# Optimization experiments

Hardware: AMD Instinct MI355X
Metric: run time of the kernel (lower is better)

The kernel has to match this reference:

```python
import jax, jax.numpy as jnp
import numpy as np

D_MODEL = 1024
NUM_HEADS = 16
NUM_KV_HEADS = 4
HEAD_DIM = D_MODEL // NUM_HEADS  # 64
KV_DIM = HEAD_DIM * NUM_KV_HEADS  # 256
B, N = 2, 2048


def setup_inputs() -> dict:
    key = jax.random.key(0)
    ks = jax.random.split(key, 7)
    std = 1.0 / np.sqrt(D_MODEL)
    return {
        "x": jax.random.normal(ks[0], (B, N, D_MODEL), dtype=jnp.float32),
        "cos": jax.random.uniform(ks[1], (N, HEAD_DIM // 2), dtype=jnp.float32),
        "sin": jax.random.uniform(ks[2], (N, HEAD_DIM // 2), dtype=jnp.float32),
        "Wq": jax.random.normal(ks[3], (D_MODEL, D_MODEL), dtype=jnp.float32) * std,
        "Wk": jax.random.normal(ks[4], (D_MODEL, KV_DIM), dtype=jnp.float32) * std,
        "Wv": jax.random.normal(ks[5], (D_MODEL, KV_DIM), dtype=jnp.float32) * std,
        "Wo": jax.random.normal(ks[6], (D_MODEL, D_MODEL), dtype=jnp.float32) * std,
    }


def _rope(t, cos, sin):
    # t: [B, H, N, head_dim]; cos/sin: [N, head_dim//2]
    t1, t2 = t[..., ::2], t[..., 1::2]
    c = cos[None, None]
    s = sin[None, None]
    # NOTE: halves are concatenated (not re-interleaved), faithful to source.
    return jnp.concatenate([t1 * c - t2 * s, t1 * s + t2 * c], axis=-1)


def reference(x, cos, sin, Wq, Wk, Wv, Wo):
    b, n, d = x.shape
    scale = HEAD_DIM ** -0.5
    q = (x @ Wq).reshape(b, n, NUM_HEADS, HEAD_DIM).transpose(0, 2, 1, 3)
    k = (x @ Wk).reshape(b, n, NUM_KV_HEADS, HEAD_DIM).transpose(0, 2, 1, 3)
    v = (x @ Wv).reshape(b, n, NUM_KV_HEADS, HEAD_DIM).transpose(0, 2, 1, 3)
    q = _rope(q, cos, sin)
    k = _rope(k, cos, sin)
    num_rep = NUM_HEADS // NUM_KV_HEADS
    k = jnp.repeat(k, num_rep, axis=1)  # [b, H, n, hd]
    v = jnp.repeat(v, num_rep, axis=1)
    attn = jnp.einsum("bhqd,bhkd->bhqk", q, k) * scale
    attn = jax.nn.softmax(attn, axis=-1)
    out = jnp.einsum("bhqk,bhkd->bhqd", attn, v)
    out = out.transpose(0, 2, 1, 3).reshape(b, n, d)
    return out @ Wo
```

## Files before the change

kernel.cpp:

```cpp
#include <hip/hip_runtime.h>
#include <math.h>

#define D_MODEL 1024
#define NHEADS  16
#define NKV     4
#define HDIM    64
#define KVDIM   256
#define BB      2
#define NN      2048
#define MROWS   (BB*NN)
#define QKVN    1536
#define NTASK   (MROWS*NHEADS)
#define NSPLIT  4

typedef unsigned short ushort_t;
typedef unsigned int uint_t;
typedef float    f32x4 __attribute__((ext_vector_type(4)));
typedef _Float16 h16x8 __attribute__((ext_vector_type(8)));
typedef __fp16   fp16x2 __attribute__((ext_vector_type(2)));

#define MFMAH(A,B,C) __builtin_amdgcn_mfma_f32_16x16x32_f16((A),(B),(C),0,0,0)

#define GLDS(gp, lp) __builtin_amdgcn_global_load_lds( \
    (const __attribute__((address_space(1))) void*)(gp), \
    (__attribute__((address_space(3))) void*)(lp), 16, 0, 0)

__device__ __forceinline__ ushort_t f2h(float f) {
    _Float16 h = (_Float16)f;
    return *(ushort_t*)&h;
}
__device__ __forceinline__ float h2f(ushort_t u) {
    return (float)(*(const _Float16*)&u);
}
__device__ __forceinline__ uint_t pk2h(float a, float b) {
    fp16x2 v = __builtin_amdgcn_cvt_pkrtz(a, b);
    return *(uint_t*)&v;
}

__global__ __launch_bounds__(256)
void cast_kernel(const float* __restrict__ src, ushort_t* __restrict__ dst, int n4)
{
    int i = blockIdx.x * 256 + threadIdx.x;
    if (i >= n4) return;
    float4 v = ((const float4*)src)[i];
    uint2 o;
    o.x = pk2h(v.x, v.y);
    o.y = pk2h(v.z, v.w);
    ((uint2*)dst)[i] = o;
}

__global__ __launch_bounds__(256)
void transpose_cast(const float* __restrict__ src, ushort_t* __restrict__ dst,
                    int K, int N)
{
    __shared__ float T[32][33];
    const int tx = threadIdx.x & 31, ty = threadIdx.x >> 5;
    const int n0 = blockIdx.x * 32, k0 = blockIdx.y * 32;
#pragma unroll
    for (int i = 0; i < 4; i++)
        T[ty + i * 8][tx] = src[(size_t)(k0 + ty + i * 8) * N + n0 + tx];
    __syncthreads();
#pragma unroll
    for (int i = 0; i < 4; i++)
        dst[(size_t)(n0 + ty + i * 8) * K + k0 + tx] = f2h(T[tx][ty + i * 8]);
}

__global__ __launch_bounds__(256)
void vtrans_kernel(const ushort_t* __restrict__ QKVh, ushort_t* __restrict__ Vt)
{
    __shared__ ushort_t T[32][34];
    const int tx = threadIdx.x & 31, ty = threadIdx.x >> 5;
    const int n0 = blockIdx.x * 32, d0 = blockIdx.y * 32, b = blockIdx.z;
#pragma unroll
    for (int i = 0; i < 4; i++)
        T[ty + i * 8][tx] =
            QKVh[(size_t)(b * NN + n0 + ty + i * 8) * QKVN + 1280 + d0 + tx];
    __syncthreads();
#pragma unroll
    for (int i = 0; i < 4; i++)
        Vt[(size_t)(b * 256 + d0 + ty + i * 8) * NN + n0 + tx] = T[tx][ty + i * 8];
}

#define NQW (MROWS*NHEADS*32)
#define NKW (MROWS*NKV*32)
__global__ __launch_bounds__(256)
void rope_kernel(const ushort_t* __restrict__ QKVh, const float* __restrict__ Cos,
                 const float* __restrict__ Sin, ushort_t* __restrict__ Qb,
                 ushort_t* __restrict__ Kb)
{
    const float SC = 0.125f * 1.44269504f;
    int idx = blockIdx.x * 256 + threadIdx.x;
    if (idx < NQW) {
        const int row = idx >> 9, rem = idx & 511;
        const int h = rem >> 5, j = rem & 31;
        const int b = row >> 11, n = row & (NN - 1);
        const uint_t pr = *(const uint_t*)&QKVh[(size_t)row * QKVN + h * 64 + 2 * j];
        const float e = h2f((ushort_t)pr), o = h2f((ushort_t)(pr >> 16));
        const float c = Cos[n * 32 + j], s = Sin[n * 32 + j];
        ushort_t* dst = Qb + ((size_t)(b * 16 + h) * NN + n) * 64;
        dst[j]      = f2h((e * c - o * s) * SC);
        dst[j + 32] = f2h((e * s + o * c) * SC);
    } else {
        const int i2 = idx - NQW;
        const int row = i2 >> 7, rem = i2 & 127;
        const int h = rem >> 5, j = rem & 31;
        const int b = row >> 11, n = row & (NN - 1);
        const uint_t pr = *(const uint_t*)&QKVh[(size_t)row * QKVN + 1024 + h * 64 + 2 * j];
        const float e = h2f((ushort_t)pr), o = h2f((ushort_t)(pr >> 16));
        const float c = Cos[n * 32 + j], s = Sin[n * 32 + j];
        ushort_t* dst = Kb + ((size_t)(b * 4 + h) * NN + n) * 64;
        dst[j]      = f2h(e * c - o * s);
        dst[j + 32] = f2h(e * s + o * c);
    }
}

__global__ __launch_bounds__(256)
void gemm_bt(const ushort_t* __restrict__ A, const ushort_t* __restrict__ Bt,
             void* __restrict__ C, int M, int N, int K, int halfout)
{
    __shared__ ushort_t As[2][128 * 32];
    __shared__ ushort_t Bs[2][64 * 32];

    const int tid  = threadIdx.x;
    const int wave = tid >> 6, lane = tid & 63;
    const int quad = lane >> 4, l16 = lane & 15;
    const int rowBase = blockIdx.y * 128, colBase = blockIdx.x * 64;
    const int wm = (wave >> 1) * 64, wn = (wave & 1) * 32;

    f32x4 acc[4][2];
    const f32x4 zz = {0.f, 0.f, 0.f, 0.f};
#pragma unroll
    for (int i = 0; i < 4; i++)
#pragma unroll
        for (int j = 0; j < 2; j++) acc[i][j] = zz;

    const int sr = wave * 32 + (lane >> 2);
    const int sc = ((lane & 3) ^ ((lane >> 3) & 3)) * 8;
    const ushort_t* Ag0 = A + (size_t)(rowBase + sr) * K + sc;
    const ushort_t* Ag1 = A + (size_t)(rowBase + sr + 16) * K + sc;
    const int segA0 = (wave * 2 + 0) * 512, segA1 = (wave * 2 + 1) * 512;
    const int br = wave * 16 + (lane >> 2);
    const ushort_t* Bg0 = Bt + (size_t)(colBase + br) * K + sc;
    const int segB = wave * 512;

    const int fcol = (quad ^ ((l16 >> 1) & 3)) * 8;

    GLDS(Ag0, &As[0][segA0]);
    GLDS(Ag1, &As[0][segA1]);
    GLDS(Bg0, &Bs[0][segB]);

    for (int k0 = 0; k0 < K; k0 += 32) {
        const int cur = (k0 >> 5) & 1, nxt = cur ^ 1;
        __syncthreads();
        if (k0 + 32 < K) {
            GLDS(Ag0 + k0 + 32, &As[nxt][segA0]);
            GLDS(Ag1 + k0 + 32, &As[nxt][segA1]);
            GLDS(Bg0 + k0 + 32, &Bs[nxt][segB]);
        }

        h16x8 af[4], bf[2];
#pragma unroll
        for (int mt = 0; mt < 4; mt++)
            af[mt] = *(const h16x8*)&As[cur][(wm + mt * 16 + l16) * 32 + fcol];
#pragma unroll
        for (int nt = 0; nt < 2; nt++)
            bf[nt] = *(const h16x8*)&Bs[cur][(wn + nt * 16 + l16) * 32 + fcol];
#pragma unroll
        for (int mt = 0; mt < 4; mt++)
#pragma unroll
            for (int nt = 0; nt < 2; nt++)
                acc[mt][nt] = MFMAH(af[mt], bf[nt], acc[mt][nt]);
    }

    if (halfout) {
        ushort_t* Ch = (ushort_t*)C;
#pragma unroll
        for (int mt = 0; mt < 4; mt++)
#pragma unroll
            for (int nt = 0; nt < 2; nt++) {
                const int row = rowBase + wm + mt * 16 + quad * 4;
                const int col = colBase + wn + nt * 16 + l16;
#pragma unroll
                for (int r = 0; r < 4; r++)
                    Ch[(size_t)(row + r) * N + col] = f2h(acc[mt][nt][r]);
            }
    } else {
        float* Cf = (float*)C;
#pragma unroll
        for (int mt = 0; mt < 4; mt++)
#pragma unroll
            for (int nt = 0; nt < 2; nt++) {
                const int row = rowBase + wm + mt * 16 + quad * 4;
                const int col = colBase + wn + nt * 16 + l16;
#pragma unroll
                for (int r = 0; r < 4; r++)
                    Cf[(size_t)(row + r) * N + col] = acc[mt][nt][r];
            }
    }
}

__global__ __launch_bounds__(256)
void attn_mfma(const ushort_t* __restrict__ Qb, const ushort_t* __restrict__ Kb,
               const ushort_t* __restrict__ Vt, ushort_t* __restrict__ Pnum,
               float* __restrict__ Pl)
{
    const int qt = blockIdx.x, h = blockIdx.y;
    const int b = blockIdx.z >> 2, chunk = blockIdx.z & 3;
    const int kvh = h >> 2;
    const int tid = threadIdx.x;
    const int wave = tid >> 6, lane = tid & 63;
    const int quad = lane >> 4, l16 = lane & 15;

    __shared__ ushort_t Ks[64][72];
    __shared__ ushort_t Vs[64][72];
    __shared__ ushort_t Ps[4][16 * 72];
    ushort_t* ps = &Ps[wave][0];

    const int row0 = qt * 256 + wave * 64;
    h16x8 qf[4][2];
#pragma unroll
    for (int mt = 0; mt < 4; mt++) {
        const ushort_t* qp =
            Qb + ((size_t)(b * 16 + h) * NN + row0 + mt * 16 + l16) * 64 + quad * 8;
        qf[mt][0] = *(const h16x8*)qp;
        qf[mt][1] = *(const h16x8*)(qp + 32);
    }

    const ushort_t* kbase = Kb + (size_t)(b * 4 + kvh) * NN * 64;
    const ushort_t* vbase = Vt + (size_t)(b * 256 + kvh * 64) * NN;
    const int key_lo = chunk * (NN / NSPLIT);
    const int rot = (qt + ((h & 3) << 1)) & 7;

    const int srow = tid >> 2, sseg = (tid & 3) * 8;

    const f32x4 zz = {0.f, 0.f, 0.f, 0.f};
    f32x4 o[4][4];
#pragma unroll
    for (int mt = 0; mt < 4; mt++)
#pragma unroll
        for (int dt = 0; dt < 4; dt++) o[mt][dt] = zz;
    float lacc[4] = {0.f, 0.f, 0.f, 0.f};

    int key0 = key_lo + rot * 64;
    const ushort_t* kp0 = kbase + (size_t)(key0 + srow) * 64 + sseg;
    const ushort_t* vp0 = vbase + (size_t)srow * NN + key0 + sseg;
    uint4 kreg0 = *(const uint4*)kp0;
    uint4 kreg1 = *(const uint4*)(kp0 + 32);
    uint4 vreg0 = *(const uint4*)vp0;
    uint4 vreg1 = *(const uint4*)(vp0 + 32);

    for (int t = 0; t < 8; t++) {
        __syncthreads();
        *(uint4*)&Ks[srow][sseg]      = kreg0;
        *(uint4*)&Ks[srow][sseg + 32] = kreg1;
        *(uint4*)&Vs[srow][sseg]      = vreg0;
        *(uint4*)&Vs[srow][sseg + 32] = vreg1;
        __syncthreads();

        if (t < 7) {
            const int kn = key_lo + ((rot + t + 1) & 7) * 64;
            const ushort_t* kpn = kbase + (size_t)(kn + srow) * 64 + sseg;
            const ushort_t* vpn = vbase + (size_t)srow * NN + kn + sseg;
            kreg0 = *(const uint4*)kpn;
            kreg1 = *(const uint4*)(kpn + 32);
            vreg0 = *(const uint4*)vpn;
            vreg1 = *(const uint4*)(vpn + 32);
        }

        uint2 pkreg[4][4];
#pragma unroll
        for (int kt = 0; kt < 4; kt++) {
            h16x8 kf0 = *(const h16x8*)&Ks[kt * 16 + l16][quad * 8];
            h16x8 kf1 = *(const h16x8*)&Ks[kt * 16 + l16][32 + quad * 8];
#pragma unroll
            for (int mt = 0; mt < 4; mt++) {
                f32x4 st = MFMAH(kf0, qf[mt][0], zz);
                st = MFMAH(kf1, qf[mt][1], st);
                const float p0 = exp2f(st[0]);
                const float p1 = exp2f(st[1]);
                const float p2 = exp2f(st[2]);
                const float p3 = exp2f(st[3]);
                lacc[mt] += (p0 + p1) + (p2 + p3);
                pkreg[kt][mt].x = pk2h(p0, p1);
                pkreg[kt][mt].y = pk2h(p2, p3);
            }
        }

        h16x8 vf[4][2];
#pragma unroll
        for (int dt = 0; dt < 4; dt++) {
            vf[dt][0] = *(const h16x8*)&Vs[dt * 16 + l16][quad * 8];
            vf[dt][1] = *(const h16x8*)&Vs[dt * 16 + l16][32 + quad * 8];
        }
#pragma unroll
        for (int mt = 0; mt < 4; mt++) {
#pragma unroll
            for (int kt = 0; kt < 4; kt++)
                *(uint2*)&ps[l16 * 72 + kt * 16 + quad * 4] = pkreg[kt][mt];
            h16x8 pa0 = *(const h16x8*)&ps[l16 * 72 + quad * 8];
            h16x8 pa1 = *(const h16x8*)&ps[l16 * 72 + 32 + quad * 8];
#pragma unroll
            for (int dt = 0; dt < 4; dt++) {
                o[mt][dt] = MFMAH(vf[dt][0], pa0, o[mt][dt]);
                o[mt][dt] = MFMAH(vf[dt][1], pa1, o[mt][dt]);
            }
        }
    }

#pragma unroll
    for (int mt = 0; mt < 4; mt++) {
        lacc[mt] += __shfl_xor(lacc[mt], 16, 64);
        lacc[mt] += __shfl_xor(lacc[mt], 32, 64);
    }

    const size_t task0 = (size_t)(b * 16 + h) * NN + row0;
    ushort_t* np = Pnum + ((size_t)chunk * NTASK + task0) * 64;
#pragma unroll
    for (int mt = 0; mt < 4; mt++) {
        const float inv = 1.0f / lacc[mt];
#pragma unroll
        for (int dt = 0; dt < 4; dt++) {
            f32x4 v = o[mt][dt];
            uint2 pk;
            pk.x = pk2h(v[0] * inv, v[1] * inv);
            pk.y = pk2h(v[2] * inv, v[3] * inv);
            *(uint2*)&np[(size_t)(mt * 16 + l16) * 64 + dt * 16 + quad * 4] = pk;
        }
        if (quad == 0)
            Pl[(size_t)chunk * NTASK + task0 + mt * 16 + l16] = lacc[mt];
    }
}

__global__ __launch_bounds__(256)
void attn_combine(const ushort_t* __restrict__ Pnum, const float* __restrict__ Pl,
                  ushort_t* __restrict__ Ob)
{
    const int gid  = blockIdx.x * 256 + threadIdx.x;
    const int task = gid >> 4;
    const int d    = (gid & 15) * 4;
    float a0 = 0.f, a1 = 0.f, a2 = 0.f, a3 = 0.f, lsum = 0.f;
#pragma unroll
    for (int s = 0; s < NSPLIT; s++) {
        const uint2 pk = *(const uint2*)&Pnum[((size_t)s * NTASK + task) * 64 + d];
        const float l = Pl[(size_t)s * NTASK + task];
        const fp16x2 lo = *(const fp16x2*)&pk.x;
        const fp16x2 hi = *(const fp16x2*)&pk.y;
        a0 += l * (float)lo.x; a1 += l * (float)lo.y;
        a2 += l * (float)hi.x; a3 += l * (float)hi.y;
        lsum += l;
    }
    const float inv = 1.0f / lsum;
    const int n = task & (NN - 1), bh = task >> 11;
    const int h = bh & (NHEADS - 1), b = bh >> 4;
    ushort_t* op = Ob + (size_t)(b * NN + n) * D_MODEL + h * 64 + d;
    uint2 o2;
    o2.x = pk2h(a0 * inv, a1 * inv);
    o2.y = pk2h(a2 * inv, a3 * inv);
    *(uint2*)op = o2;
}

extern "C" void kernel_launch(void* const* d_in, const int* in_sizes, int n_in,
                              void* d_out, int out_size, void* d_ws, size_t ws_size,
                              hipStream_t stream)
{
    const float* x    = (const float*)d_in[0];
    const float* cosp = (const float*)d_in[1];
    const float* sinp = (const float*)d_in[2];
    const float* Wq   = (const float*)d_in[3];
    const float* Wk   = (const float*)d_in[4];
    const float* Wv   = (const float*)d_in[5];
    const float* Wo   = (const float*)d_in[6];

    char* w = (char*)d_ws;
    ushort_t* xb     = (ushort_t*)w;                       w += (size_t)MROWS * D_MODEL * 2;
    ushort_t* WqkvT  = (ushort_t*)w;                       w += (size_t)QKVN * D_MODEL * 2;
    ushort_t* WoT    = (ushort_t*)w;                       w += (size_t)D_MODEL * D_MODEL * 2;
    ushort_t* QKVh   = (ushort_t*)w;                       w += (size_t)MROWS * QKVN * 2;
    ushort_t* Qbuf   = (ushort_t*)w;                       w += (size_t)MROWS * D_MODEL * 2;
    ushort_t* Kbuf   = (ushort_t*)w;                       w += (size_t)MROWS * KVDIM * 2;
    ushort_t* Vt     = (ushort_t*)w;                       w += (size_t)MROWS * KVDIM * 2;
    ushort_t* Obuf   = (ushort_t*)w;                       w += (size_t)MROWS * D_MODEL * 2;
    ushort_t* Pnum   = (ushort_t*)w;                       w += (size_t)NSPLIT * NTASK * 64 * 2;
    float*    Pl     = (float*)w;

    cast_kernel<<<(MROWS * D_MODEL / 4 + 255) / 256, 256, 0, stream>>>(
        x, xb, MROWS * D_MODEL / 4);
    transpose_cast<<<dim3(D_MODEL / 32, D_MODEL / 32), 256, 0, stream>>>(
        Wq, WqkvT, D_MODEL, D_MODEL);
    transpose_cast<<<dim3(KVDIM / 32, D_MODEL / 32), 256, 0, stream>>>(
        Wk, WqkvT + (size_t)1024 * D_MODEL, D_MODEL, KVDIM);
    transpose_cast<<<dim3(KVDIM / 32, D_MODEL / 32), 256, 0, stream>>>(
        Wv, WqkvT + (size_t)1280 * D_MODEL, D_MODEL, KVDIM);
    transpose_cast<<<dim3(D_MODEL / 32, D_MODEL / 32), 256, 0, stream>>>(
        Wo, WoT, D_MODEL, D_MODEL);

    gemm_bt<<<dim3(QKVN / 64, MROWS / 128), 256, 0, stream>>>(
        xb, WqkvT, QKVh, MROWS, QKVN, D_MODEL, 1);

    rope_kernel<<<(NQW + NKW) / 256, 256, 0, stream>>>(QKVh, cosp, sinp, Qbuf, Kbuf);
    vtrans_kernel<<<dim3(NN / 32, KVDIM / 32, BB), 256, 0, stream>>>(QKVh, Vt);

    attn_mfma<<<dim3(NN / 256, NHEADS, BB * NSPLIT), 256, 0, stream>>>(
        Qbuf, Kbuf, Vt, Pnum, Pl);
    attn_combine<<<(NTASK * 16) / 256, 256, 0, stream>>>(Pnum, Pl, Obuf);

    gemm_bt<<<dim3(D_MODEL / 64, MROWS / 128), 256, 0, stream>>>(
        Obuf, WoT, d_out, MROWS, D_MODEL, D_MODEL, 0);
}
```

Measured before the change: 216.6 us.

## Fuse split-KV combine into Wo GEMM, merge prep kernels, halve KV splits

Merges the five cast and transpose launches into one prep kernel dispatched by block index. Halves the split-KV count, so each attention block covers twice as many keys and there are half as many partial outputs. Removes the separate combine kernel and the O buffer: the Wo GEMM now loads both partial numerators and their weights, normalizes and converts them to fp16 in registers, and stores the result into padded shared memory as its A tile. This cuts launch overhead and an intermediate round trip through global memory, at the cost of less attention parallelism and redundant combine work repeated across the GEMM's column blocks.

```diff
diff --git a/kernel.cpp b/kernel.cpp
--- a/kernel.cpp
+++ b/kernel.cpp
@@ -11,7 +11,7 @@
 #define MROWS   (BB*NN)
 #define QKVN    1536
 #define NTASK   (MROWS*NHEADS)
-#define NSPLIT  4
+#define NSPLIT  2
 
 typedef unsigned short ushort_t;
 typedef unsigned int uint_t;
@@ -38,31 +38,37 @@
 }
 
 __global__ __launch_bounds__(256)
-void cast_kernel(const float* __restrict__ src, ushort_t* __restrict__ dst, int n4)
-{
-    int i = blockIdx.x * 256 + threadIdx.x;
-    if (i >= n4) return;
-    float4 v = ((const float4*)src)[i];
-    uint2 o;
-    o.x = pk2h(v.x, v.y);
-    o.y = pk2h(v.z, v.w);
-    ((uint2*)dst)[i] = o;
-}
-
-__global__ __launch_bounds__(256)
-void transpose_cast(const float* __restrict__ src, ushort_t* __restrict__ dst,
-                    int K, int N)
+void prep_kernel(const float* __restrict__ x, const float* __restrict__ Wq,
+                 const float* __restrict__ Wk, const float* __restrict__ Wv,
+                 const float* __restrict__ Wo, ushort_t* __restrict__ xb,
+                 ushort_t* __restrict__ WqkvT, ushort_t* __restrict__ WoT)
 {
     __shared__ float T[32][33];
+    int blk = blockIdx.x;
+    if (blk < 4096) {
+        const int i = blk * 256 + threadIdx.x;
+        float4 v = ((const float4*)x)[i];
+        uint2 o;
+        o.x = pk2h(v.x, v.y);
+        o.y = pk2h(v.z, v.w);
+        ((uint2*)xb)[i] = o;
+        return;
+    }
+    blk -= 4096;
+    const float* src; ushort_t* dst; int N, bx, by;
+    if (blk < 1024)      { src = Wq; dst = WqkvT;                            N = D_MODEL; bx = blk & 31; by = blk >> 5; }
+    else if (blk < 1280) { blk -= 1024; src = Wk; dst = WqkvT + (size_t)1024 * D_MODEL; N = KVDIM; bx = blk & 7; by = blk >> 3; }
+    else if (blk < 1536) { blk -= 1280; src = Wv; dst = WqkvT + (size_t)1280 * D_MODEL; N = KVDIM; bx = blk & 7; by = blk >> 3; }
+    else                 { blk -= 1536; src = Wo; dst = WoT;                 N = D_MODEL; bx = blk & 31; by = blk >> 5; }
     const int tx = threadIdx.x & 31, ty = threadIdx.x >> 5;
-    const int n0 = blockIdx.x * 32, k0 = blockIdx.y * 32;
+    const int n0 = bx * 32, k0 = by * 32;
 #pragma unroll
     for (int i = 0; i < 4; i++)
         T[ty + i * 8][tx] = src[(size_t)(k0 + ty + i * 8) * N + n0 + tx];
     __syncthreads();
 #pragma unroll
     for (int i = 0; i < 4; i++)
-        dst[(size_t)(n0 + ty + i * 8) * K + k0 + tx] = f2h(T[tx][ty + i * 8]);
+        dst[(size_t)(n0 + ty + i * 8) * D_MODEL + k0 + tx] = f2h(T[tx][ty + i * 8]);
 }
 
 __global__ __launch_bounds__(256)
@@ -115,8 +121,8 @@
 }
 
 __global__ __launch_bounds__(256)
-void gemm_bt(const ushort_t* __restrict__ A, const ushort_t* __restrict__ Bt,
-             void* __restrict__ C, int M, int N, int K, int halfout)
+void gemm_qkv(const ushort_t* __restrict__ A, const ushort_t* __restrict__ Bt,
+              ushort_t* __restrict__ C, int M, int N, int K)
 {
     __shared__ ushort_t As[2][128 * 32];
     __shared__ ushort_t Bs[2][64 * 32];
@@ -172,31 +178,16 @@
                 acc[mt][nt] = MFMAH(af[mt], bf[nt], acc[mt][nt]);
     }
 
-    if (halfout) {
-        ushort_t* Ch = (ushort_t*)C;
-#pragma unroll
-        for (int mt = 0; mt < 4; mt++)
-#pragma unroll
-            for (int nt = 0; nt < 2; nt++) {
-                const int row = rowBase + wm + mt * 16 + quad * 4;
-                const int col = colBase + wn + nt * 16 + l16;
-#pragma unroll
-                for (int r = 0; r < 4; r++)
-                    Ch[(size_t)(row + r) * N + col] = f2h(acc[mt][nt][r]);
-            }
-    } else {
-        float* Cf = (float*)C;
-#pragma unroll
-        for (int mt = 0; mt < 4; mt++)
-#pragma unroll
-            for (int nt = 0; nt < 2; nt++) {
-                const int row = rowBase + wm + mt * 16 + quad * 4;
-                const int col = colBase + wn + nt * 16 + l16;
-#pragma unroll
-                for (int r = 0; r < 4; r++)
-                    Cf[(size_t)(row + r) * N + col] = acc[mt][nt][r];
-            }
-    }
+#pragma unroll
+    for (int mt = 0; mt < 4; mt++)
+#pragma unroll
+        for (int nt = 0; nt < 2; nt++) {
+            const int row = rowBase + wm + mt * 16 + quad * 4;
+            const int col = colBase + wn + nt * 16 + l16;
+#pragma unroll
+            for (int r = 0; r < 4; r++)
+                C[(size_t)(row + r) * N + col] = f2h(acc[mt][nt][r]);
+        }
 }
 
 __global__ __launch_bounds__(256)
@@ -205,7 +196,7 @@
                float* __restrict__ Pl)
 {
     const int qt = blockIdx.x, h = blockIdx.y;
-    const int b = blockIdx.z >> 2, chunk = blockIdx.z & 3;
+    const int b = blockIdx.z >> 1, chunk = blockIdx.z & 1;
     const int kvh = h >> 2;
     const int tid = threadIdx.x;
     const int wave = tid >> 6, lane = tid & 63;
@@ -229,7 +220,7 @@
     const ushort_t* kbase = Kb + (size_t)(b * 4 + kvh) * NN * 64;
     const ushort_t* vbase = Vt + (size_t)(b * 256 + kvh * 64) * NN;
     const int key_lo = chunk * (NN / NSPLIT);
-    const int rot = (qt + ((h & 3) << 1)) & 7;
+    const int rot = (qt + ((h & 3) << 2)) & 15;
 
     const int srow = tid >> 2, sseg = (tid & 3) * 8;
 
@@ -249,7 +240,7 @@
     uint4 vreg0 = *(const uint4*)vp0;
     uint4 vreg1 = *(const uint4*)(vp0 + 32);
 
-    for (int t = 0; t < 8; t++) {
+    for (int t = 0; t < 16; t++) {
         __syncthreads();
         *(uint4*)&Ks[srow][sseg]      = kreg0;
         *(uint4*)&Ks[srow][sseg + 32] = kreg1;
@@ -257,8 +248,8 @@
         *(uint4*)&Vs[srow][sseg + 32] = vreg1;
         __syncthreads();
 
-        if (t < 7) {
-            const int kn = key_lo + ((rot + t + 1) & 7) * 64;
+        if (t < 15) {
+            const int kn = key_lo + ((rot + t + 1) & 15) * 64;
             const ushort_t* kpn = kbase + (size_t)(kn + srow) * 64 + sseg;
             const ushort_t* vpn = vbase + (size_t)srow * NN + kn + sseg;
             kreg0 = *(const uint4*)kpn;
@@ -332,31 +323,114 @@
 }
 
 __global__ __launch_bounds__(256)
-void attn_combine(const ushort_t* __restrict__ Pnum, const float* __restrict__ Pl,
-                  ushort_t* __restrict__ Ob)
-{
-    const int gid  = blockIdx.x * 256 + threadIdx.x;
-    const int task = gid >> 4;
-    const int d    = (gid & 15) * 4;
-    float a0 = 0.f, a1 = 0.f, a2 = 0.f, a3 = 0.f, lsum = 0.f;
-#pragma unroll
-    for (int s = 0; s < NSPLIT; s++) {
-        const uint2 pk = *(const uint2*)&Pnum[((size_t)s * NTASK + task) * 64 + d];
-        const float l = Pl[(size_t)s * NTASK + task];
-        const fp16x2 lo = *(const fp16x2*)&pk.x;
-        const fp16x2 hi = *(const fp16x2*)&pk.y;
-        a0 += l * (float)lo.x; a1 += l * (float)lo.y;
-        a2 += l * (float)hi.x; a3 += l * (float)hi.y;
-        lsum += l;
-    }
-    const float inv = 1.0f / lsum;
-    const int n = task & (NN - 1), bh = task >> 11;
-    const int h = bh & (NHEADS - 1), b = bh >> 4;
-    ushort_t* op = Ob + (size_t)(b * NN + n) * D_MODEL + h * 64 + d;
-    uint2 o2;
-    o2.x = pk2h(a0 * inv, a1 * inv);
-    o2.y = pk2h(a2 * inv, a3 * inv);
-    *(uint2*)op = o2;
+void gemm_wo(const ushort_t* __restrict__ Pnum, const float* __restrict__ Pl,
+             const ushort_t* __restrict__ WoT, float* __restrict__ C)
+{
+    __shared__ ushort_t As[2][128 * 40];
+    __shared__ ushort_t Bs[2][64 * 32];
+
+    const int tid  = threadIdx.x;
+    const int wave = tid >> 6, lane = tid & 63;
+    const int quad = lane >> 4, l16 = lane & 15;
+    const int rowBase = blockIdx.y * 128, colBase = blockIdx.x * 64;
+    const int wm = (wave >> 1) * 64, wn = (wave & 1) * 32;
+
+    f32x4 acc[4][2];
+    const f32x4 zz = {0.f, 0.f, 0.f, 0.f};
+#pragma unroll
+    for (int i = 0; i < 4; i++)
+#pragma unroll
+        for (int j = 0; j < 2; j++) acc[i][j] = zz;
+
+    const int r0 = tid >> 2;
+    const int c8 = (tid & 3) * 8;
+    const int bB = rowBase >> 11;
+    const int n0 = (rowBase & (NN - 1)) + r0;
+
+    const int br = wave * 16 + (lane >> 2);
+    const int sc = ((lane & 3) ^ ((lane >> 3) & 3)) * 8;
+    const ushort_t* Bg0 = WoT + (size_t)(colBase + br) * D_MODEL + sc;
+    const int segB = wave * 512;
+    const int fcol = (quad ^ ((l16 >> 1) & 3)) * 8;
+
+    uint4 a0c0, a0c1, a1c0, a1c1;
+    float l00, l01, l10, l11;
+#define PREFA(k0) { \
+        const int h_ = (k0) >> 6; \
+        const int d_ = ((k0) & 63) + c8; \
+        const size_t t0_ = ((size_t)(bB * 16 + h_) << 11) + n0; \
+        const size_t t1_ = t0_ + 64; \
+        a0c0 = *(const uint4*)&Pnum[t0_ * 64 + d_]; \
+        a0c1 = *(const uint4*)&Pnum[((size_t)NTASK + t0_) * 64 + d_]; \
+        a1c0 = *(const uint4*)&Pnum[t1_ * 64 + d_]; \
+        a1c1 = *(const uint4*)&Pnum[((size_t)NTASK + t1_) * 64 + d_]; \
+        l00 = Pl[t0_]; l01 = Pl[NTASK + t0_]; \
+        l10 = Pl[t1_]; l11 = Pl[NTASK + t1_]; \
+    }
+
+    PREFA(0);
+    GLDS(Bg0, &Bs[0][segB]);
+
+    for (int k0 = 0; k0 < D_MODEL; k0 += 32) {
+        const int cur = (k0 >> 5) & 1, nxt = cur ^ 1;
+        __syncthreads();
+
+        {
+            const float i0 = 1.f / (l00 + l01), w00 = l00 * i0, w01 = l01 * i0;
+            const float i1 = 1.f / (l10 + l11), w10 = l10 * i1, w11 = l11 * i1;
+            uint4 o0, o1;
+            const uint_t* p0 = (const uint_t*)&a0c0;
+            const uint_t* p1 = (const uint_t*)&a0c1;
+            const uint_t* q0 = (const uint_t*)&a1c0;
+            const uint_t* q1 = (const uint_t*)&a1c1;
+            uint_t* po = (uint_t*)&o0;
+            uint_t* qo = (uint_t*)&o1;
+#pragma unroll
+            for (int j = 0; j < 4; j++) {
+                fp16x2 u = *(const fp16x2*)&p0[j];
+                fp16x2 v = *(const fp16x2*)&p1[j];
+                po[j] = pk2h(w00 * (float)u.x + w01 * (float)v.x,
+                             w00 * (float)u.y + w01 * (float)v.y);
+                fp16x2 s = *(const fp16x2*)&q0[j];
+                fp16x2 r = *(const fp16x2*)&q1[j];
+                qo[j] = pk2h(w10 * (float)s.x + w11 * (float)r.x,
+                             w10 * (float)s.y + w11 * (float)r.y);
+            }
+            *(uint4*)&As[cur][r0 * 40 + c8]        = o0;
+            *(uint4*)&As[cur][(r0 + 64) * 40 + c8] = o1;
+        }
+        __syncthreads();
+
+        if (k0 + 32 < D_MODEL) {
+            GLDS(Bg0 + k0 + 32, &Bs[nxt][segB]);
+            PREFA(k0 + 32);
+        }
+
+        h16x8 af[4], bf[2];
+#pragma unroll
+        for (int mt = 0; mt < 4; mt++)
+            af[mt] = *(const h16x8*)&As[cur][(wm + mt * 16 + l16) * 40 + quad * 8];
+#pragma unroll
+        for (int nt = 0; nt < 2; nt++)
+            bf[nt] = *(const h16x8*)&Bs[cur][(wn + nt * 16 + l16) * 32 + fcol];
+#pragma unroll
+        for (int mt = 0; mt < 4; mt++)
+#pragma unroll
+            for (int nt = 0; nt < 2; nt++)
+                acc[mt][nt] = MFMAH(af[mt], bf[nt], acc[mt][nt]);
+    }
+#undef PREFA
+
+#pragma unroll
+    for (int mt = 0; mt < 4; mt++)
+#pragma unroll
+        for (int nt = 0; nt < 2; nt++) {
+            const int row = rowBase + wm + mt * 16 + quad * 4;
+            const int col = colBase + wn + nt * 16 + l16;
+#pragma unroll
+            for (int r = 0; r < 4; r++)
+                C[(size_t)(row + r) * D_MODEL + col] = acc[mt][nt][r];
+        }
 }
 
 extern "C" void kernel_launch(void* const* d_in, const int* in_sizes, int n_in,
@@ -379,31 +453,20 @@
     ushort_t* Qbuf   = (ushort_t*)w;                       w += (size_t)MROWS * D_MODEL * 2;
     ushort_t* Kbuf   = (ushort_t*)w;                       w += (size_t)MROWS * KVDIM * 2;
     ushort_t* Vt     = (ushort_t*)w;                       w += (size_t)MROWS * KVDIM * 2;
-    ushort_t* Obuf   = (ushort_t*)w;                       w += (size_t)MROWS * D_MODEL * 2;
     ushort_t* Pnum   = (ushort_t*)w;                       w += (size_t)NSPLIT * NTASK * 64 * 2;
     float*    Pl     = (float*)w;
 
-    cast_kernel<<<(MROWS * D_MODEL / 4 + 255) / 256, 256, 0, stream>>>(
-        x, xb, MROWS * D_MODEL / 4);
-    transpose_cast<<<dim3(D_MODEL / 32, D_MODEL / 32), 256, 0, stream>>>(
-        Wq, WqkvT, D_MODEL, D_MODEL);
-    transpose_cast<<<dim3(KVDIM / 32, D_MODEL / 32), 256, 0, stream>>>(
-        Wk, WqkvT + (size_t)1024 * D_MODEL, D_MODEL, KVDIM);
-    transpose_cast<<<dim3(KVDIM / 32, D_MODEL / 32), 256, 0, stream>>>(
-        Wv, WqkvT + (size_t)1280 * D_MODEL, D_MODEL, KVDIM);
-    transpose_cast<<<dim3(D_MODEL / 32, D_MODEL / 32), 256, 0, stream>>>(
-        Wo, WoT, D_MODEL, D_MODEL);
-
-    gemm_bt<<<dim3(QKVN / 64, MROWS / 128), 256, 0, stream>>>(
-        xb, WqkvT, QKVh, MROWS, QKVN, D_MODEL, 1);
+    prep_kernel<<<6656, 256, 0, stream>>>(x, Wq, Wk, Wv, Wo, xb, WqkvT, WoT);
+
+    gemm_qkv<<<dim3(QKVN / 64, MROWS / 128), 256, 0, stream>>>(
+        xb, WqkvT, QKVh, MROWS, QKVN, D_MODEL);
 
     rope_kernel<<<(NQW + NKW) / 256, 256, 0, stream>>>(QKVh, cosp, sinp, Qbuf, Kbuf);
     vtrans_kernel<<<dim3(NN / 32, KVDIM / 32, BB), 256, 0, stream>>>(QKVh, Vt);
 
     attn_mfma<<<dim3(NN / 256, NHEADS, BB * NSPLIT), 256, 0, stream>>>(
         Qbuf, Kbuf, Vt, Pnum, Pl);
-    attn_combine<<<(NTASK * 16) / 256, 256, 0, stream>>>(Pnum, Pl, Obuf);
-
-    gemm_bt<<<dim3(D_MODEL / 64, MROWS / 128), 256, 0, stream>>>(
-        Obuf, WoT, d_out, MROWS, D_MODEL, D_MODEL, 0);
-}
+
+    gemm_wo<<<dim3(D_MODEL / 64, MROWS / 128), 256, 0, stream>>>(
+        Pnum, Pl, WoT, (float*)d_out);
+}
```

Measured after the change: 215.4 us. About the same (-0.5%).
